# Performance work log

Hardware: AMD Instinct MI355X
Metric: run time of the kernel (lower is better)

The kernel has to match this reference:

```python
import jax, jax.numpy as jnp
import numpy as np
from jax import lax

RADIUS = 8
EPS = 1e-3
EPS_LOG = 1e-6
EPS_SCALE = 1e-4
A_COMP = 0.7
B_SHIFT = 0.0
DETAIL_GAIN = 1.0
DOWN = 0.5
# detail_threshold=0 and target_mean=0 -> those branches are inactive (defaults)

DN = (('NCHW', 'OIHW', 'NCHW'))


def _box_filter(x4d):
    """Separable box filter on [1,1,H,W] with reflect padding, kernel 2r+1."""
    k = 2 * RADIUS + 1
    xp = jnp.pad(x4d, ((0, 0), (0, 0), (RADIUS, RADIUS), (RADIUS, RADIUS)), mode='reflect')
    kh = jnp.full((1, 1, 1, k), 1.0 / k, dtype=x4d.dtype)
    kv = jnp.full((1, 1, k, 1), 1.0 / k, dtype=x4d.dtype)
    y = lax.conv_general_dilated(xp, kh, (1, 1), 'VALID', dimension_numbers=DN)
    y = lax.conv_general_dilated(y, kv, (1, 1), 'VALID', dimension_numbers=DN)
    return y


def _guided_filter(img):
    """Self-guided filter on a 2D image [H, W]."""
    x4 = img[None, None]
    mean_I = _box_filter(x4)
    mean_II = _box_filter(x4 * x4)
    var_I = mean_II - mean_I * mean_I
    a = var_I / (var_I + EPS)
    b = mean_I - a * mean_I
    out = _box_filter(a) * x4 + _box_filter(b)
    return out[0, 0]


def _bilinear_resize(img, oh, ow):
    """Bilinear resize [H,W] -> [oh,ow], half-pixel centers (align_corners=False),
    no antialias, matching torch F.interpolate(mode='bilinear')."""
    H, W = img.shape
    ys = jnp.maximum((jnp.arange(oh, dtype=img.dtype) + 0.5) * (H / oh) - 0.5, 0.0)
    xs = jnp.maximum((jnp.arange(ow, dtype=img.dtype) + 0.5) * (W / ow) - 0.5, 0.0)
    y0 = jnp.floor(ys)
    x0 = jnp.floor(xs)
    wy = (ys - y0)[:, None]
    wx = (xs - x0)[None, :]
    y0i = jnp.clip(y0.astype(jnp.int32), 0, H - 1)
    y1i = jnp.minimum(y0i + 1, H - 1)
    x0i = jnp.clip(x0.astype(jnp.int32), 0, W - 1)
    x1i = jnp.minimum(x0i + 1, W - 1)
    # vertical lerp, then horizontal lerp (separable)
    vert = img[y0i, :] * (1.0 - wy) + img[y1i, :] * wy       # [oh, W]
    out = vert[:, x0i] * (1.0 - wx) + vert[:, x1i] * wx      # [oh, ow]
    return out


def setup_inputs() -> dict:
    key = jax.random.key(0)
    x = jax.random.uniform(key, (2160, 3840, 3), dtype=jnp.float32)
    return {"x": x}


def reference(x) -> jnp.ndarray:
    H, W = x.shape[0], x.shape[1]
    Y = 0.2126 * x[..., 0] + 0.7152 * x[..., 1] + 0.0722 * x[..., 2]
    Y_log = jnp.log2(jnp.maximum(Y, EPS_LOG))
    # fast path: downsample -> guided filter -> upsample
    dh, dw = int(H * DOWN), int(W * DOWN)
    Y_log_down = _bilinear_resize(Y_log, dh, dw)
    Y_base_down = _guided_filter(Y_log_down)
    Y_base = _bilinear_resize(Y_base_down, H, W)
    Y_detail = Y_log - Y_base  # detail_threshold=0 -> no suppression
    Y_tm = (A_COMP * Y_base + B_SHIFT) + DETAIL_GAIN * Y_detail
    Y_out = jnp.exp2(Y_tm)
    scale = Y_out / (Y + EPS_SCALE)
    out = jnp.clip(x * scale[..., None], 0.0, 1.0)
    # target_mean=0 -> no global mean rescale
    return out
```

## Files before the change

### kernel.cpp

```cpp
#include <hip/hip_runtime.h>
#include <math.h>

#define H_FULL 2160
#define W_FULL 3840
#define H_D    1080
#define W_D    1920
#define KLEN   17
#define INV_K2 (1.0f/289.0f)

#if __has_builtin(__builtin_amdgcn_logf)
#define FAST_LOG2(x) __builtin_amdgcn_logf(x)
#else
#define FAST_LOG2(x) log2f(x)
#endif
#if __has_builtin(__builtin_amdgcn_exp2f)
#define FAST_EXP2(x) __builtin_amdgcn_exp2f(x)
#else
#define FAST_EXP2(x) exp2f(x)
#endif
#if __has_builtin(__builtin_amdgcn_rcpf)
#define FAST_RCP(x) __builtin_amdgcn_rcpf(x)
#else
#define FAST_RCP(x) (1.0f/(x))
#endif

static __device__ __forceinline__ int refl(int i, int n) {
    if (i < 0) i = -i;
    else if (i >= n) i = 2*n - 2 - i;
    return i;
}
static __device__ __forceinline__ float lum(float r, float g, float b) {
    return 0.2126f*r + 0.7152f*g + 0.0722f*b;
}
static __device__ __forceinline__ float lg(float y) {
    return FAST_LOG2(fmaxf(y, 1e-6f));
}

__global__ __launch_bounds__(256) void k_down(const float* __restrict__ x,
                                              float* __restrict__ I) {
    int t = blockIdx.x * 256 + threadIdx.x;
    int p = t * 2;
    int i = p / W_D;
    int j = p - i * W_D;
    const float4* r0 = (const float4*)(x + ((size_t)(2*i)   * W_FULL + 2*j) * 3);
    const float4* r1 = (const float4*)(x + ((size_t)(2*i+1) * W_FULL + 2*j) * 3);
    float4 a0 = r0[0], a1 = r0[1], a2 = r0[2];
    float4 b0 = r1[0], b1 = r1[1], b2 = r1[2];
    float y00 = lum(a0.x,a0.y,a0.z), y01 = lum(a0.w,a1.x,a1.y);
    float y02 = lum(a1.z,a1.w,a2.x), y03 = lum(a2.y,a2.z,a2.w);
    float y10 = lum(b0.x,b0.y,b0.z), y11 = lum(b0.w,b1.x,b1.y);
    float y12 = lum(b1.z,b1.w,b2.x), y13 = lum(b2.y,b2.z,b2.w);
    float o0 = 0.25f * (lg(y00)+lg(y01)+lg(y10)+lg(y11));
    float o1 = 0.25f * (lg(y02)+lg(y03)+lg(y12)+lg(y13));
    *(float2*)(I + (size_t)i * W_D + j) = make_float2(o0, o1);
}

__global__ __launch_bounds__(512, 6) void k_filter(const float* __restrict__ I,
                                                   float* __restrict__ base) {
    __shared__ char lds[52088];
    float*  sIc   = (float*) (lds);
    float*  sIf   = (float*) (lds + 4760);
    float2* ab    = (float2*)(lds + 4760);
    float2* hI    = (float2*)(lds + 25160);
    float2* hab   = (float2*)(lds + 25160);
    float*  baseL = (float*) (lds + 39160);

    int tx0 = blockIdx.x * 32;
    int ty0 = blockIdx.y * 32;
    int tid = threadIdx.x;

    for (int e = tid; e < 66 * 66; e += 512) {
        int r = e / 66, c = e - r * 66;
        sIf[r * 67 + c] =
            I[(size_t)refl(ty0 - 17 + r, H_D) * W_D + refl(tx0 - 17 + c, W_D)];
    }
    __syncthreads();

    if (tid < 330) {
        int r = tid / 5, run = tid - (tid / 5) * 5;
        int c0 = run * 10;
        const float* p = &sIf[r * 67 + c0];
        float s1 = 0.f, s2 = 0.f;
        #pragma unroll
        for (int k = 0; k < KLEN; ++k) { float v = p[k]; s1 += v; s2 += v * v; }
        float2* o = &hI[r * 51 + c0];
        o[0] = make_float2(s1, s2);
        #pragma unroll
        for (int m = 1; m < 10; ++m) {
            float vo = p[m - 1], vi = p[m + 16];
            s1 += vi - vo;
            s2 += vi * vi - vo * vo;
            o[m] = make_float2(s1, s2);
        }
    }
    for (int e = tid; e < 34 * 34; e += 512) {
        int r = e / 34, c = e - r * 34;
        sIc[r * 35 + c] = sIf[(r + 16) * 67 + (c + 16)];
    }
    __syncthreads();

    if (tid < 250) {
        int c = tid % 50, run = tid / 50;
        int r0 = run * 10;
        const float2* p = &hI[r0 * 51 + c];
        float s1 = 0.f, s2 = 0.f;
        #pragma unroll
        for (int k = 0; k < KLEN; ++k) { float2 v = p[k * 51]; s1 += v.x; s2 += v.y; }
        float2* o = &ab[r0 * 51 + c];
        #pragma unroll
        for (int m = 0; m < 10; ++m) {
            if (m) {
                float2 vi = p[(m + 16) * 51], vo = p[(m - 1) * 51];
                s1 += vi.x - vo.x;
                s2 += vi.y - vo.y;
            }
            float mI  = s1 * INV_K2;
            float mII = s2 * INV_K2;
            float var = mII - mI * mI;
            float av  = var / (var + 1e-3f);
            o[m * 51] = make_float2(av, mI - av * mI);
        }
    }
    __syncthreads();

    if (tid < 200) {
        int r = tid % 50, run = tid / 50;
        int c0  = (run < 2) ? run * 9 : 18 + (run - 2) * 8;
        int len = (run < 2) ? 9 : 8;
        const float2* p = &ab[r * 51 + c0];
        float sa = 0.f, sb = 0.f;
        #pragma unroll
        for (int k = 0; k < KLEN; ++k) { float2 v = p[k]; sa += v.x; sb += v.y; }
        float2* o = &hab[r * 35 + c0];
        o[0] = make_float2(sa, sb);
        #pragma unroll
        for (int m = 1; m < 9; ++m) {
            if (m < len) {
                float2 vi = p[m + 16], vo = p[m - 1];
                sa += vi.x - vo.x;
                sb += vi.y - vo.y;
                o[m] = make_float2(sa, sb);
            }
        }
    }
    __syncthreads();

    if (tid < 136) {
        int cc = tid % 34, run = tid / 34;
        int r0  = (run < 2) ? run * 9 : 18 + (run - 2) * 8;
        int len = (run < 2) ? 9 : 8;
        const float2* p = &hab[r0 * 35 + cc];
        float sa = 0.f, sb = 0.f;
        #pragma unroll
        for (int k = 0; k < KLEN; ++k) { float2 v = p[k * 35]; sa += v.x; sb += v.y; }
        #pragma unroll
        for (int m = 0; m < 9; ++m) {
            if (m < len) {
                if (m) {
                    float2 vi = p[(m + 16) * 35], vo = p[(m - 1) * 35];
                    sa += vi.x - vo.x;
                    sb += vi.y - vo.y;
                }
                int br = r0 + m;
                baseL[br * 35 + cc] =
                    (sa * INV_K2) * sIc[br * 35 + cc] + sb * INV_K2;
            }
        }
    }
    __syncthreads();

    for (int e = tid; e < 32 * 32; e += 512) {
        int r = e >> 5, c = e & 31;
        int gr = ty0 + r;
        if (gr < H_D) base[(size_t)gr * W_D + (tx0 + c)] = baseL[(r + 1) * 35 + (c + 1)];
    }
}

__global__ __launch_bounds__(256) void k_tm(const float* __restrict__ x,
                                            const float* __restrict__ base,
                                            float* __restrict__ out) {
    int t = blockIdx.x * 256 + threadIdx.x;
    int oy = t / 960;
    int g  = t - oy * 960;
    int j0 = g * 4;
    int k2 = g * 2;

    int y0g = (oy - 1) >> 1;
    int y0 = max(y0g, 0);
    int y1 = min(y0g + 1, H_D - 1);
    float wy = (oy & 1) ? 0.25f : 0.75f;
    const float* b0 = base + (size_t)y0 * W_D;
    const float* b1 = base + (size_t)y1 * W_D;
    int c0 = max(k2 - 1, 0);
    int c3 = min(k2 + 2, W_D - 1);
    float u0 = b0[c0],     w0 = b1[c0];
    float u1 = b0[k2],     w1 = b1[k2];
    float u2 = b0[k2 + 1], w2 = b1[k2 + 1];
    float u3 = b0[c3],     w3 = b1[c3];
    float v0 = u0 + (w0 - u0) * wy;
    float v1 = u1 + (w1 - u1) * wy;
    float v2 = u2 + (w2 - u2) * wy;
    float v3 = u3 + (w3 - u3) * wy;
    float Yb[4];
    Yb[0] = v0 + (v1 - v0) * 0.75f;
    Yb[1] = v1 + (v2 - v1) * 0.25f;
    Yb[2] = v1 + (v2 - v1) * 0.75f;
    Yb[3] = v2 + (v3 - v2) * 0.25f;

    size_t off = ((size_t)oy * W_FULL + j0) * 3;
    const float4* px = (const float4*)(x + off);
    float4 q0 = px[0], q1 = px[1], q2 = px[2];
    float rgb[12] = {q0.x,q0.y,q0.z,q0.w, q1.x,q1.y,q1.z,q1.w, q2.x,q2.y,q2.z,q2.w};
    float res[12];
    #pragma unroll
    for (int k = 0; k < 4; ++k) {
        float rr = rgb[3*k], gg = rgb[3*k+1], bb = rgb[3*k+2];
        float Y = lum(rr, gg, bb);
        float sc = fmaxf(Y, 1e-6f) * FAST_EXP2(-0.3f * Yb[k]) * FAST_RCP(Y + 1e-4f);
        res[3*k]   = fminf(fmaxf(rr * sc, 0.f), 1.f);
        res[3*k+1] = fminf(fmaxf(gg * sc, 0.f), 1.f);
        res[3*k+2] = fminf(fmaxf(bb * sc, 0.f), 1.f);
    }
    float4* po = (float4*)(out + off);
    po[0] = make_float4(res[0], res[1], res[2],  res[3]);
    po[1] = make_float4(res[4], res[5], res[6],  res[7]);
    po[2] = make_float4(res[8], res[9], res[10], res[11]);
}

__global__ __launch_bounds__(512, 6) void k_fused(const float* __restrict__ I,
                                                  const float* __restrict__ x,
                                                  float* __restrict__ out) {
    __shared__ char lds[52088];
    float*  sIc   = (float*) (lds);
    float*  sIf   = (float*) (lds + 4760);
    float2* ab    = (float2*)(lds + 4760);
    float2* hI    = (float2*)(lds + 25160);
    float2* hab   = (float2*)(lds + 25160);
    float*  baseL = (float*) (lds + 39160);

    int tx0 = blockIdx.x * 32;
    int ty0 = blockIdx.y * 32;
    int tid = threadIdx.x;

    for (int e = tid; e < 66 * 66; e += 512) {
        int r = e / 66, c = e - r * 66;
        sIf[r * 67 + c] =
            I[(size_t)refl(ty0 - 17 + r, H_D) * W_D + refl(tx0 - 17 + c, W_D)];
    }
    __syncthreads();

    if (tid < 330) {
        int r = tid / 5, run = tid - (tid / 5) * 5;
        int c0 = run * 10;
        const float* p = &sIf[r * 67 + c0];
        float s1 = 0.f, s2 = 0.f;
        #pragma unroll
        for (int k = 0; k < KLEN; ++k) { float v = p[k]; s1 += v; s2 += v * v; }
        float2* o = &hI[r * 51 + c0];
        o[0] = make_float2(s1, s2);
        #pragma unroll
        for (int m = 1; m < 10; ++m) {
            float vo = p[m - 1], vi = p[m + 16];
            s1 += vi - vo;
            s2 += vi * vi - vo * vo;
            o[m] = make_float2(s1, s2);
        }
    }
    for (int e = tid; e < 34 * 34; e += 512) {
        int r = e / 34, c = e - r * 34;
        sIc[r * 35 + c] = sIf[(r + 16) * 67 + (c + 16)];
    }
    __syncthreads();

    if (tid < 250) {
        int c = tid % 50, run = tid / 50;
        int r0 = run * 10;
        const float2* p = &hI[r0 * 51 + c];
        float s1 = 0.f, s2 = 0.f;
        #pragma unroll
        for (int k = 0; k < KLEN; ++k) { float2 v = p[k * 51]; s1 += v.x; s2 += v.y; }
        float2* o = &ab[r0 * 51 + c];
        #pragma unroll
        for (int m = 0; m < 10; ++m) {
            if (m) {
                float2 vi = p[(m + 16) * 51], vo = p[(m - 1) * 51];
                s1 += vi.x - vo.x;
                s2 += vi.y - vo.y;
            }
            float mI  = s1 * INV_K2;
            float mII = s2 * INV_K2;
            float var = mII - mI * mI;
            float av  = var / (var + 1e-3f);
            o[m * 51] = make_float2(av, mI - av * mI);
        }
    }
    __syncthreads();

    if (tid < 200) {
        int r = tid % 50, run = tid / 50;
        int c0  = (run < 2) ? run * 9 : 18 + (run - 2) * 8;
        int len = (run < 2) ? 9 : 8;
        const float2* p = &ab[r * 51 + c0];
        float sa = 0.f, sb = 0.f;
        #pragma unroll
        for (int k = 0; k < KLEN; ++k) { float2 v = p[k]; sa += v.x; sb += v.y; }
        float2* o = &hab[r * 35 + c0];
        o[0] = make_float2(sa, sb);
        #pragma unroll
        for (int m = 1; m < 9; ++m) {
            if (m < len) {
                float2 vi = p[m + 16], vo = p[m - 1];
                sa += vi.x - vo.x;
                sb += vi.y - vo.y;
                o[m] = make_float2(sa, sb);
            }
        }
    }
    __syncthreads();

    if (tid < 136) {
        int cc = tid % 34, run = tid / 34;
        int r0  = (run < 2) ? run * 9 : 18 + (run - 2) * 8;
        int len = (run < 2) ? 9 : 8;
        const float2* p = &hab[r0 * 35 + cc];
        float sa = 0.f, sb = 0.f;
        #pragma unroll
        for (int k = 0; k < KLEN; ++k) { float2 v = p[k * 35]; sa += v.x; sb += v.y; }
        #pragma unroll
        for (int m = 0; m < 9; ++m) {
            if (m < len) {
                if (m) {
                    float2 vi = p[(m + 16) * 35], vo = p[(m - 1) * 35];
                    sa += vi.x - vo.x;
                    sb += vi.y - vo.y;
                }
                int br = r0 + m;
                baseL[br * 35 + cc] =
                    (sa * INV_K2) * sIc[br * 35 + cc] + sb * INV_K2;
            }
        }
    }
    __syncthreads();

    int q  = tid & 15;
    int r  = tid >> 4;
    int j0 = tx0 * 2 + q * 4;
    int gc0 = tx0 + 2 * q - 1;
    int l0 = max(gc0, 0) - (tx0 - 1);
    int l1 = 2 * q + 1, l2 = 2 * q + 2;
    int l3 = min(gc0 + 3, W_D - 1) - (tx0 - 1);

    #pragma unroll
    for (int s = 0; s < 2; ++s) {
        int oy = ty0 * 2 + r + s * 32;
        if (oy < H_FULL) {
            int y0g = (oy - 1) >> 1;
            int ly0 = max(y0g, 0) - (ty0 - 1);
            int ly1 = min(y0g + 1, H_D - 1) - (ty0 - 1);
            float wy = (oy & 1) ? 0.25f : 0.75f;
            const float* b0r = &baseL[ly0 * 35];
            const float* b1r = &baseL[ly1 * 35];
            float v0 = b0r[l0] + (b1r[l0] - b0r[l0]) * wy;
            float v1 = b0r[l1] + (b1r[l1] - b0r[l1]) * wy;
            float v2 = b0r[l2] + (b1r[l2] - b0r[l2]) * wy;
            float v3 = b0r[l3] + (b1r[l3] - b0r[l3]) * wy;
            float Yb[4];
            Yb[0] = v0 + (v1 - v0) * 0.75f;
            Yb[1] = v1 + (v2 - v1) * 0.25f;
            Yb[2] = v1 + (v2 - v1) * 0.75f;
            Yb[3] = v2 + (v3 - v2) * 0.25f;

            size_t off = ((size_t)oy * W_FULL + j0) * 3;
            const float4* px = (const float4*)(x + off);
            float4 q0 = px[0], q1 = px[1], q2 = px[2];
            float rgb[12] = {q0.x,q0.y,q0.z,q0.w, q1.x,q1.y,q1.z,q1.w, q2.x,q2.y,q2.z,q2.w};
            float res[12];
            #pragma unroll
            for (int k = 0; k < 4; ++k) {
                float rr = rgb[3*k], gg = rgb[3*k+1], bb = rgb[3*k+2];
                float Y = lum(rr, gg, bb);
                float sc = fmaxf(Y, 1e-6f) * FAST_EXP2(-0.3f * Yb[k]) * FAST_RCP(Y + 1e-4f);
                res[3*k]   = fminf(fmaxf(rr * sc, 0.f), 1.f);
                res[3*k+1] = fminf(fmaxf(gg * sc, 0.f), 1.f);
                res[3*k+2] = fminf(fmaxf(bb * sc, 0.f), 1.f);
            }
            float4* po = (float4*)(out + off);
            po[0] = make_float4(res[0], res[1], res[2],  res[3]);
            po[1] = make_float4(res[4], res[5], res[6],  res[7]);
            po[2] = make_float4(res[8], res[9], res[10], res[11]);
        }
    }
}

extern "C" void kernel_launch(void* const* d_in, const int* in_sizes, int n_in,
                              void* d_out, int out_size, void* d_ws, size_t ws_size,
                              hipStream_t stream) {
    (void)in_sizes; (void)n_in; (void)out_size;
    const float* x = (const float*)d_in[0];
    float* out = (float*)d_out;
    float* I = (float*)d_ws;
    size_t plane = (size_t)H_D * W_D;

    if (ws_size >= 2 * plane * sizeof(float)) {
        float* base = I + plane;
        k_down  <<<dim3(4050, 1, 1), dim3(256, 1, 1), 0, stream>>>(x, I);
        k_filter<<<dim3(60, 34, 1),  dim3(512, 1, 1), 0, stream>>>(I, base);
        k_tm    <<<dim3(8100, 1, 1), dim3(256, 1, 1), 0, stream>>>(x, base, out);
    } else {
        k_down  <<<dim3(4050, 1, 1), dim3(256, 1, 1), 0, stream>>>(x, I);
        k_fused <<<dim3(60, 34, 1),  dim3(512, 1, 1), 0, stream>>>(I, x, out);
    }
}
```

Measured before the change: 80.48 us.

## Split guided filter into a/b pass and fused second-box-plus-tonemap pass

Replaces the filter and tonemap kernels with two kernels. The first computes the per-pixel a/b coefficients over a 48x48 halo tile and writes them to a float2 workspace. The second reads a 50x50 tile of a/b plus a small I tile, applies the second box filter, and tonemaps the full-resolution pixels directly from LDS, so the base plane is no longer written out and read back. This removes the wide 66x66 halo and its redundant first-pass box work and drops the separate base round trip, in exchange for writing and reading an 8-byte-per-pixel a/b plane and needing a larger workspace.

```diff
diff --git a/kernel.cpp b/kernel.cpp
--- a/kernel.cpp
+++ b/kernel.cpp
@@ -55,62 +55,51 @@
     *(float2*)(I + (size_t)i * W_D + j) = make_float2(o0, o1);
 }
 
-__global__ __launch_bounds__(512, 6) void k_filter(const float* __restrict__ I,
-                                                   float* __restrict__ base) {
-    __shared__ char lds[52088];
-    float*  sIc   = (float*) (lds);
-    float*  sIf   = (float*) (lds + 4760);
-    float2* ab    = (float2*)(lds + 4760);
-    float2* hI    = (float2*)(lds + 25160);
-    float2* hab   = (float2*)(lds + 25160);
-    float*  baseL = (float*) (lds + 39160);
-
+__global__ __launch_bounds__(256) void k_ab(const float* __restrict__ I,
+                                            float2* __restrict__ AB) {
+    __shared__ float  sI[48 * 49];
+    __shared__ float2 hs[48 * 33];
     int tx0 = blockIdx.x * 32;
     int ty0 = blockIdx.y * 32;
     int tid = threadIdx.x;
 
-    for (int e = tid; e < 66 * 66; e += 512) {
-        int r = e / 66, c = e - r * 66;
-        sIf[r * 67 + c] =
-            I[(size_t)refl(ty0 - 17 + r, H_D) * W_D + refl(tx0 - 17 + c, W_D)];
-    }
-    __syncthreads();
-
-    if (tid < 330) {
-        int r = tid / 5, run = tid - (tid / 5) * 5;
-        int c0 = run * 10;
-        const float* p = &sIf[r * 67 + c0];
+    for (int e = tid; e < 48 * 48; e += 256) {
+        int r = e / 48, c = e - r * 48;
+        sI[r * 49 + c] =
+            I[(size_t)refl(ty0 - 8 + r, H_D) * W_D + refl(tx0 - 8 + c, W_D)];
+    }
+    __syncthreads();
+
+    if (tid < 192) {
+        int r = tid >> 2, run = tid & 3;
+        int c0 = run * 8;
+        const float* p = &sI[r * 49 + c0];
         float s1 = 0.f, s2 = 0.f;
         #pragma unroll
         for (int k = 0; k < KLEN; ++k) { float v = p[k]; s1 += v; s2 += v * v; }
-        float2* o = &hI[r * 51 + c0];
+        float2* o = &hs[r * 33 + c0];
         o[0] = make_float2(s1, s2);
         #pragma unroll
-        for (int m = 1; m < 10; ++m) {
+        for (int m = 1; m < 8; ++m) {
             float vo = p[m - 1], vi = p[m + 16];
             s1 += vi - vo;
             s2 += vi * vi - vo * vo;
             o[m] = make_float2(s1, s2);
         }
     }
-    for (int e = tid; e < 34 * 34; e += 512) {
-        int r = e / 34, c = e - r * 34;
-        sIc[r * 35 + c] = sIf[(r + 16) * 67 + (c + 16)];
-    }
-    __syncthreads();
-
-    if (tid < 250) {
-        int c = tid % 50, run = tid / 50;
-        int r0 = run * 10;
-        const float2* p = &hI[r0 * 51 + c];
+    __syncthreads();
+
+    if (tid < 128) {
+        int c = tid & 31, run = tid >> 5;
+        int r0 = run * 8;
+        const float2* p = &hs[r0 * 33 + c];
         float s1 = 0.f, s2 = 0.f;
         #pragma unroll
-        for (int k = 0; k < KLEN; ++k) { float2 v = p[k * 51]; s1 += v.x; s2 += v.y; }
-        float2* o = &ab[r0 * 51 + c];
-        #pragma unroll
-        for (int m = 0; m < 10; ++m) {
+        for (int k = 0; k < KLEN; ++k) { float2 v = p[k * 33]; s1 += v.x; s2 += v.y; }
+        #pragma unroll
+        for (int m = 0; m < 8; ++m) {
             if (m) {
-                float2 vi = p[(m + 16) * 51], vo = p[(m - 1) * 51];
+                float2 vi = p[(m + 16) * 33], vo = p[(m - 1) * 33];
                 s1 += vi.x - vo.x;
                 s2 += vi.y - vo.y;
             }
@@ -118,8 +107,36 @@
             float mII = s2 * INV_K2;
             float var = mII - mI * mI;
             float av  = var / (var + 1e-3f);
-            o[m * 51] = make_float2(av, mI - av * mI);
-        }
+            int gr = ty0 + r0 + m;
+            if (gr < H_D)
+                AB[(size_t)gr * W_D + tx0 + c] = make_float2(av, mI - av * mI);
+        }
+    }
+}
+
+__global__ __launch_bounds__(512, 6) void k_fused2(const float* __restrict__ I,
+                                                   const float2* __restrict__ AB,
+                                                   const float* __restrict__ x,
+                                                   float* __restrict__ out) {
+    __shared__ char lds[39160];
+    float2* sAB   = (float2*)(lds);
+    float2* hAB   = (float2*)(lds + 20400);
+    float*  sIc   = (float*) (lds + 34400);
+    float*  baseL = (float*) (lds);
+
+    int tx0 = blockIdx.x * 32;
+    int ty0 = blockIdx.y * 32;
+    int tid = threadIdx.x;
+
+    for (int e = tid; e < 50 * 50; e += 512) {
+        int r = e / 50, c = e - r * 50;
+        sAB[r * 51 + c] =
+            AB[(size_t)refl(ty0 - 9 + r, H_D) * W_D + refl(tx0 - 9 + c, W_D)];
+    }
+    for (int e = tid; e < 34 * 34; e += 512) {
+        int r = e / 34, c = e - r * 34;
+        sIc[r * 35 + c] =
+            I[(size_t)refl(ty0 - 1 + r, H_D) * W_D + refl(tx0 - 1 + c, W_D)];
     }
     __syncthreads();
 
@@ -127,11 +144,11 @@
         int r = tid % 50, run = tid / 50;
         int c0  = (run < 2) ? run * 9 : 18 + (run - 2) * 8;
         int len = (run < 2) ? 9 : 8;
-        const float2* p = &ab[r * 51 + c0];
+        const float2* p = &sAB[r * 51 + c0];
         float sa = 0.f, sb = 0.f;
         #pragma unroll
         for (int k = 0; k < KLEN; ++k) { float2 v = p[k]; sa += v.x; sb += v.y; }
-        float2* o = &hab[r * 35 + c0];
+        float2* o = &hAB[r * 35 + c0];
         o[0] = make_float2(sa, sb);
         #pragma unroll
         for (int m = 1; m < 9; ++m) {
@@ -149,180 +166,7 @@
         int cc = tid % 34, run = tid / 34;
         int r0  = (run < 2) ? run * 9 : 18 + (run - 2) * 8;
         int len = (run < 2) ? 9 : 8;
-        const float2* p = &hab[r0 * 35 + cc];
-        float sa = 0.f, sb = 0.f;
-        #pragma unroll
-        for (int k = 0; k < KLEN; ++k) { float2 v = p[k * 35]; sa += v.x; sb += v.y; }
-        #pragma unroll
-        for (int m = 0; m < 9; ++m) {
-            if (m < len) {
-                if (m) {
-                    float2 vi = p[(m + 16) * 35], vo = p[(m - 1) * 35];
-                    sa += vi.x - vo.x;
-                    sb += vi.y - vo.y;
-                }
-                int br = r0 + m;
-                baseL[br * 35 + cc] =
-                    (sa * INV_K2) * sIc[br * 35 + cc] + sb * INV_K2;
-            }
-        }
-    }
-    __syncthreads();
-
-    for (int e = tid; e < 32 * 32; e += 512) {
-        int r = e >> 5, c = e & 31;
-        int gr = ty0 + r;
-        if (gr < H_D) base[(size_t)gr * W_D + (tx0 + c)] = baseL[(r + 1) * 35 + (c + 1)];
-    }
-}
-
-__global__ __launch_bounds__(256) void k_tm(const float* __restrict__ x,
-                                            const float* __restrict__ base,
-                                            float* __restrict__ out) {
-    int t = blockIdx.x * 256 + threadIdx.x;
-    int oy = t / 960;
-    int g  = t - oy * 960;
-    int j0 = g * 4;
-    int k2 = g * 2;
-
-    int y0g = (oy - 1) >> 1;
-    int y0 = max(y0g, 0);
-    int y1 = min(y0g + 1, H_D - 1);
-    float wy = (oy & 1) ? 0.25f : 0.75f;
-    const float* b0 = base + (size_t)y0 * W_D;
-    const float* b1 = base + (size_t)y1 * W_D;
-    int c0 = max(k2 - 1, 0);
-    int c3 = min(k2 + 2, W_D - 1);
-    float u0 = b0[c0],     w0 = b1[c0];
-    float u1 = b0[k2],     w1 = b1[k2];
-    float u2 = b0[k2 + 1], w2 = b1[k2 + 1];
-    float u3 = b0[c3],     w3 = b1[c3];
-    float v0 = u0 + (w0 - u0) * wy;
-    float v1 = u1 + (w1 - u1) * wy;
-    float v2 = u2 + (w2 - u2) * wy;
-    float v3 = u3 + (w3 - u3) * wy;
-    float Yb[4];
-    Yb[0] = v0 + (v1 - v0) * 0.75f;
-    Yb[1] = v1 + (v2 - v1) * 0.25f;
-    Yb[2] = v1 + (v2 - v1) * 0.75f;
-    Yb[3] = v2 + (v3 - v2) * 0.25f;
-
-    size_t off = ((size_t)oy * W_FULL + j0) * 3;
-    const float4* px = (const float4*)(x + off);
-    float4 q0 = px[0], q1 = px[1], q2 = px[2];
-    float rgb[12] = {q0.x,q0.y,q0.z,q0.w, q1.x,q1.y,q1.z,q1.w, q2.x,q2.y,q2.z,q2.w};
-    float res[12];
-    #pragma unroll
-    for (int k = 0; k < 4; ++k) {
-        float rr = rgb[3*k], gg = rgb[3*k+1], bb = rgb[3*k+2];
-        float Y = lum(rr, gg, bb);
-        float sc = fmaxf(Y, 1e-6f) * FAST_EXP2(-0.3f * Yb[k]) * FAST_RCP(Y + 1e-4f);
-        res[3*k]   = fminf(fmaxf(rr * sc, 0.f), 1.f);
-        res[3*k+1] = fminf(fmaxf(gg * sc, 0.f), 1.f);
-        res[3*k+2] = fminf(fmaxf(bb * sc, 0.f), 1.f);
-    }
-    float4* po = (float4*)(out + off);
-    po[0] = make_float4(res[0], res[1], res[2],  res[3]);
-    po[1] = make_float4(res[4], res[5], res[6],  res[7]);
-    po[2] = make_float4(res[8], res[9], res[10], res[11]);
-}
-
-__global__ __launch_bounds__(512, 6) void k_fused(const float* __restrict__ I,
-                                                  const float* __restrict__ x,
-                                                  float* __restrict__ out) {
-    __shared__ char lds[52088];
-    float*  sIc   = (float*) (lds);
-    float*  sIf   = (float*) (lds + 4760);
-    float2* ab    = (float2*)(lds + 4760);
-    float2* hI    = (float2*)(lds + 25160);
-    float2* hab   = (float2*)(lds + 25160);
-    float*  baseL = (float*) (lds + 39160);
-
-    int tx0 = blockIdx.x * 32;
-    int ty0 = blockIdx.y * 32;
-    int tid = threadIdx.x;
-
-    for (int e = tid; e < 66 * 66; e += 512) {
-        int r = e / 66, c = e - r * 66;
-        sIf[r * 67 + c] =
-            I[(size_t)refl(ty0 - 17 + r, H_D) * W_D + refl(tx0 - 17 + c, W_D)];
-    }
-    __syncthreads();
-
-    if (tid < 330) {
-        int r = tid / 5, run = tid - (tid / 5) * 5;
-        int c0 = run * 10;
-        const float* p = &sIf[r * 67 + c0];
-        float s1 = 0.f, s2 = 0.f;
-        #pragma unroll
-        for (int k = 0; k < KLEN; ++k) { float v = p[k]; s1 += v; s2 += v * v; }
-        float2* o = &hI[r * 51 + c0];
-        o[0] = make_float2(s1, s2);
-        #pragma unroll
-        for (int m = 1; m < 10; ++m) {
-            float vo = p[m - 1], vi = p[m + 16];
-            s1 += vi - vo;
-            s2 += vi * vi - vo * vo;
-            o[m] = make_float2(s1, s2);
-        }
-    }
-    for (int e = tid; e < 34 * 34; e += 512) {
-        int r = e / 34, c = e - r * 34;
-        sIc[r * 35 + c] = sIf[(r + 16) * 67 + (c + 16)];
-    }
-    __syncthreads();
-
-    if (tid < 250) {
-        int c = tid % 50, run = tid / 50;
-        int r0 = run * 10;
-        const float2* p = &hI[r0 * 51 + c];
-        float s1 = 0.f, s2 = 0.f;
-        #pragma unroll
-        for (int k = 0; k < KLEN; ++k) { float2 v = p[k * 51]; s1 += v.x; s2 += v.y; }
-        float2* o = &ab[r0 * 51 + c];
-        #pragma unroll
-        for (int m = 0; m < 10; ++m) {
-            if (m) {
-                float2 vi = p[(m + 16) * 51], vo = p[(m - 1) * 51];
-                s1 += vi.x - vo.x;
-                s2 += vi.y - vo.y;
-            }
-            float mI  = s1 * INV_K2;
-            float mII = s2 * INV_K2;
-            float var = mII - mI * mI;
-            float av  = var / (var + 1e-3f);
-            o[m * 51] = make_float2(av, mI - av * mI);
-        }
-    }
-    __syncthreads();
-
-    if (tid < 200) {
-        int r = tid % 50, run = tid / 50;
-        int c0  = (run < 2) ? run * 9 : 18 + (run - 2) * 8;
-        int len = (run < 2) ? 9 : 8;
-        const float2* p = &ab[r * 51 + c0];
-        float sa = 0.f, sb = 0.f;
-        #pragma unroll
-        for (int k = 0; k < KLEN; ++k) { float2 v = p[k]; sa += v.x; sb += v.y; }
-        float2* o = &hab[r * 35 + c0];
-        o[0] = make_float2(sa, sb);
-        #pragma unroll
-        for (int m = 1; m < 9; ++m) {
-            if (m < len) {
-                float2 vi = p[m + 16], vo = p[m - 1];
-                sa += vi.x - vo.x;
-                sb += vi.y - vo.y;
-                o[m] = make_float2(sa, sb);
-            }
-        }
-    }
-    __syncthreads();
-
-    if (tid < 136) {
-        int cc = tid % 34, run = tid / 34;
-        int r0  = (run < 2) ? run * 9 : 18 + (run - 2) * 8;
-        int len = (run < 2) ? 9 : 8;
-        const float2* p = &hab[r0 * 35 + cc];
+        const float2* p = &hAB[r0 * 35 + cc];
         float sa = 0.f, sb = 0.f;
         #pragma unroll
         for (int k = 0; k < KLEN; ++k) { float2 v = p[k * 35]; sa += v.x; sb += v.y; }
@@ -392,6 +236,171 @@
     }
 }
 
+__global__ __launch_bounds__(512, 6) void k_fused(const float* __restrict__ I,
+                                                  const float* __restrict__ x,
+                                                  float* __restrict__ out) {
+    __shared__ char lds[52088];
+    float*  sIc   = (float*) (lds);
+    float*  sIf   = (float*) (lds + 4760);
+    float2* ab    = (float2*)(lds + 4760);
+    float2* hI    = (float2*)(lds + 25160);
+    float2* hab   = (float2*)(lds + 25160);
+    float*  baseL = (float*) (lds + 39160);
+
+    int tx0 = blockIdx.x * 32;
+    int ty0 = blockIdx.y * 32;
+    int tid = threadIdx.x;
+
+    for (int e = tid; e < 66 * 66; e += 512) {
+        int r = e / 66, c = e - r * 66;
+        sIf[r * 67 + c] =
+            I[(size_t)refl(ty0 - 17 + r, H_D) * W_D + refl(tx0 - 17 + c, W_D)];
+    }
+    __syncthreads();
+
+    if (tid < 330) {
+        int r = tid / 5, run = tid - (tid / 5) * 5;
+        int c0 = run * 10;
+        const float* p = &sIf[r * 67 + c0];
+        float s1 = 0.f, s2 = 0.f;
+        #pragma unroll
+        for (int k = 0; k < KLEN; ++k) { float v = p[k]; s1 += v; s2 += v * v; }
+        float2* o = &hI[r * 51 + c0];
+        o[0] = make_float2(s1, s2);
+        #pragma unroll
+        for (int m = 1; m < 10; ++m) {
+            float vo = p[m - 1], vi = p[m + 16];
+            s1 += vi - vo;
+            s2 += vi * vi - vo * vo;
+            o[m] = make_float2(s1, s2);
+        }
+    }
+    for (int e = tid; e < 34 * 34; e += 512) {
+        int r = e / 34, c = e - r * 34;
+        sIc[r * 35 + c] = sIf[(r + 16) * 67 + (c + 16)];
+    }
+    __syncthreads();
+
+    if (tid < 250) {
+        int c = tid % 50, run = tid / 50;
+        int r0 = run * 10;
+        const float2* p = &hI[r0 * 51 + c];
+        float s1 = 0.f, s2 = 0.f;
+        #pragma unroll
+        for (int k = 0; k < KLEN; ++k) { float2 v = p[k * 51]; s1 += v.x; s2 += v.y; }
+        float2* o = &ab[r0 * 51 + c];
+        #pragma unroll
+        for (int m = 0; m < 10; ++m) {
+            if (m) {
+                float2 vi = p[(m + 16) * 51], vo = p[(m - 1) * 51];
+                s1 += vi.x - vo.x;
+                s2 += vi.y - vo.y;
+            }
+            float mI  = s1 * INV_K2;
+            float mII = s2 * INV_K2;
+            float var = mII - mI * mI;
+            float av  = var / (var + 1e-3f);
+            o[m * 51] = make_float2(av, mI - av * mI);
+        }
+    }
+    __syncthreads();
+
+    if (tid < 200) {
+        int r = tid % 50, run = tid / 50;
+        int c0  = (run < 2) ? run * 9 : 18 + (run - 2) * 8;
+        int len = (run < 2) ? 9 : 8;
+        const float2* p = &ab[r * 51 + c0];
+        float sa = 0.f, sb = 0.f;
+        #pragma unroll
+        for (int k = 0; k < KLEN; ++k) { float2 v = p[k]; sa += v.x; sb += v.y; }
+        float2* o = &hab[r * 35 + c0];
+        o[0] = make_float2(sa, sb);
+        #pragma unroll
+        for (int m = 1; m < 9; ++m) {
+            if (m < len) {
+                float2 vi = p[m + 16], vo = p[m - 1];
+                sa += vi.x - vo.x;
+                sb += vi.y - vo.y;
+                o[m] = make_float2(sa, sb);
+            }
+        }
+    }
+    __syncthreads();
+
+    if (tid < 136) {
+        int cc = tid % 34, run = tid / 34;
+        int r0  = (run < 2) ? run * 9 : 18 + (run - 2) * 8;
+        int len = (run < 2) ? 9 : 8;
+        const float2* p = &hab[r0 * 35 + cc];
+        float sa = 0.f, sb = 0.f;
+        #pragma unroll
+        for (int k = 0; k < KLEN; ++k) { float2 v = p[k * 35]; sa += v.x; sb += v.y; }
+        #pragma unroll
+        for (int m = 0; m < 9; ++m) {
+            if (m < len) {
+                if (m) {
+                    float2 vi = p[(m + 16) * 35], vo = p[(m - 1) * 35];
+                    sa += vi.x - vo.x;
+                    sb += vi.y - vo.y;
+                }
+                int br = r0 + m;
+                baseL[br * 35 + cc] =
+                    (sa * INV_K2) * sIc[br * 35 + cc] + sb * INV_K2;
+            }
+        }
+    }
+    __syncthreads();
+
+    int q  = tid & 15;
+    int r  = tid >> 4;
+    int j0 = tx0 * 2 + q * 4;
+    int gc0 = tx0 + 2 * q - 1;
+    int l0 = max(gc0, 0) - (tx0 - 1);
+    int l1 = 2 * q + 1, l2 = 2 * q + 2;
+    int l3 = min(gc0 + 3, W_D - 1) - (tx0 - 1);
+
+    #pragma unroll
+    for (int s = 0; s < 2; ++s) {
+        int oy = ty0 * 2 + r + s * 32;
+        if (oy < H_FULL) {
+            int y0g = (oy - 1) >> 1;
+            int ly0 = max(y0g, 0) - (ty0 - 1);
+            int ly1 = min(y0g + 1, H_D - 1) - (ty0 - 1);
+            float wy = (oy & 1) ? 0.25f : 0.75f;
+            const float* b0r = &baseL[ly0 * 35];
+            const float* b1r = &baseL[ly1 * 35];
+            float v0 = b0r[l0] + (b1r[l0] - b0r[l0]) * wy;
+            float v1 = b0r[l1] + (b1r[l1] - b0r[l1]) * wy;
+            float v2 = b0r[l2] + (b1r[l2] - b0r[l2]) * wy;
+            float v3 = b0r[l3] + (b1r[l3] - b0r[l3]) * wy;
+            float Yb[4];
+            Yb[0] = v0 + (v1 - v0) * 0.75f;
+            Yb[1] = v1 + (v2 - v1) * 0.25f;
+            Yb[2] = v1 + (v2 - v1) * 0.75f;
+            Yb[3] = v2 + (v3 - v2) * 0.25f;
+
+            size_t off = ((size_t)oy * W_FULL + j0) * 3;
+            const float4* px = (const float4*)(x + off);
+            float4 q0 = px[0], q1 = px[1], q2 = px[2];
+            float rgb[12] = {q0.x,q0.y,q0.z,q0.w, q1.x,q1.y,q1.z,q1.w, q2.x,q2.y,q2.z,q2.w};
+            float res[12];
+            #pragma unroll
+            for (int k = 0; k < 4; ++k) {
+                float rr = rgb[3*k], gg = rgb[3*k+1], bb = rgb[3*k+2];
+                float Y = lum(rr, gg, bb);
+                float sc = fmaxf(Y, 1e-6f) * FAST_EXP2(-0.3f * Yb[k]) * FAST_RCP(Y + 1e-4f);
+                res[3*k]   = fminf(fmaxf(rr * sc, 0.f), 1.f);
+                res[3*k+1] = fminf(fmaxf(gg * sc, 0.f), 1.f);
+                res[3*k+2] = fminf(fmaxf(bb * sc, 0.f), 1.f);
+            }
+            float4* po = (float4*)(out + off);
+            po[0] = make_float4(res[0], res[1], res[2],  res[3]);
+            po[1] = make_float4(res[4], res[5], res[6],  res[7]);
+            po[2] = make_float4(res[8], res[9], res[10], res[11]);
+        }
+    }
+}
+
 extern "C" void kernel_launch(void* const* d_in, const int* in_sizes, int n_in,
                               void* d_out, int out_size, void* d_ws, size_t ws_size,
                               hipStream_t stream) {
@@ -401,11 +410,11 @@
     float* I = (float*)d_ws;
     size_t plane = (size_t)H_D * W_D;
 
-    if (ws_size >= 2 * plane * sizeof(float)) {
-        float* base = I + plane;
+    if (ws_size >= plane * 12) {
+        float2* AB = (float2*)(I + plane);
         k_down  <<<dim3(4050, 1, 1), dim3(256, 1, 1), 0, stream>>>(x, I);
-        k_filter<<<dim3(60, 34, 1),  dim3(512, 1, 1), 0, stream>>>(I, base);
-        k_tm    <<<dim3(8100, 1, 1), dim3(256, 1, 1), 0, stream>>>(x, base, out);
+        k_ab    <<<dim3(60, 34, 1),  dim3(256, 1, 1), 0, stream>>>(I, AB);
+        k_fused2<<<dim3(60, 34, 1),  dim3(512, 1, 1), 0, stream>>>(I, AB, x, out);
     } else {
         k_down  <<<dim3(4050, 1, 1), dim3(256, 1, 1), 0, stream>>>(x, I);
         k_fused <<<dim3(60, 34, 1),  dim3(512, 1, 1), 0, stream>>>(I, x, out);
```

After: 77.96 us. 3.1% less time.
